# Performance work log

Hardware: AMD Instinct MI355X
Metric: run time of the kernel (lower is better)

## Reference

```python
import jax, jax.numpy as jnp
import numpy as np

EMBED_DIM = 1024
HEAD_SIZE = 64
SEQ_LEN = 2048
BATCH = 32

def setup_inputs() -> dict:
    key = jax.random.key(0)
    kx, kk, kq, kv = jax.random.split(key, 4)
    s = 1.0 / np.sqrt(EMBED_DIM)
    x = jax.random.normal(kx, (BATCH, SEQ_LEN, EMBED_DIM), dtype=jnp.float32)
    Wk = jax.random.normal(kk, (EMBED_DIM, HEAD_SIZE), dtype=jnp.float32) * s
    Wq = jax.random.normal(kq, (EMBED_DIM, HEAD_SIZE), dtype=jnp.float32) * s
    Wv = jax.random.normal(kv, (EMBED_DIM, HEAD_SIZE), dtype=jnp.float32) * s
    return {"x": x, "Wk": Wk, "Wq": Wq, "Wv": Wv}

def reference(x, Wk, Wq, Wv):
    # x: [B,T,C]; projections (no bias, per config.bias=False)
    k = jnp.einsum('btc,ch->bth', x, Wk)
    q = jnp.einsum('btc,ch->bth', x, Wq)
    v = jnp.einsum('btc,ch->bth', x, Wv)
    # NOTE: original computes k @ q^T (rows=k positions), scaled by embed_dim**-0.5
    scale = EMBED_DIM ** (-0.5)
    wei = jnp.einsum('bih,bjh->bij', k, q) * scale  # [B,T,T]
    T = x.shape[1]
    causal = jnp.tril(jnp.ones((T, T), dtype=bool))
    wei = jnp.where(causal, wei, -jnp.inf)
    wei = jax.nn.softmax(wei, axis=-1)
    # dropout: eval mode -> identity
    return jnp.einsum('bij,bjh->bih', wei, v)
```

## Files before the change

kernel.cpp:

```cpp
#include <hip/hip_runtime.h>
#include <hip/hip_bf16.h>

#define BATCH 32
#define SEQ   2048
#define EMB   1024
#define HS    64
#define BT    (BATCH*SEQ)

typedef short s16x4 __attribute__((ext_vector_type(4)));
typedef short s16x8 __attribute__((ext_vector_type(8)));
typedef float f32x4 __attribute__((ext_vector_type(4)));
using u16 = unsigned short;

static __device__ __forceinline__ short f2bf(float f) {
  __hip_bfloat16 h = __float2bfloat16(f);
  return *reinterpret_cast<short*>(&h);
}

#define MFMA __builtin_amdgcn_mfma_f32_16x16x32_bf16

__global__ __launch_bounds__(256) void wconv_kernel(
    const float* __restrict__ Wk, const float* __restrict__ Wq,
    const float* __restrict__ Wv, short* __restrict__ Wt)
{
  const int n = blockIdx.x;
  const int w = n >> 6, h = n & 63;
  const float* Wp = (w == 0) ? Wk : (w == 1) ? Wq : Wv;
  const int k0 = threadIdx.x * 4;
  s16x4 p;
  #pragma unroll
  for (int e = 0; e < 4; ++e) p[e] = f2bf(Wp[(size_t)(k0 + e) * HS + h]);
  *(s16x4*)(Wt + (size_t)n * EMB + k0) = p;
}

__global__ __launch_bounds__(256, 4) void proj_kernel(
    const float* __restrict__ x, const short* __restrict__ Wt,
    short* __restrict__ kb, short* __restrict__ qb, short* __restrict__ vt)
{
  __shared__ __align__(16) u16 xs[64][72];
  const int tid  = threadIdx.x;
  const int row0 = blockIdx.x * 64;
  const int w  = tid >> 6, l = tid & 63;
  const int lr = l & 15, lg = l >> 4;

  f32x4 acc[4][3];
  #pragma unroll
  for (int m = 0; m < 4; ++m)
    #pragma unroll
    for (int n = 0; n < 3; ++n) acc[m][n] = f32x4{0.f, 0.f, 0.f, 0.f};

  for (int k0 = 0; k0 < EMB; k0 += 64) {
    s16x8 bw[2][3];
    #pragma unroll
    for (int kk = 0; kk < 2; ++kk)
      #pragma unroll
      for (int n = 0; n < 3; ++n)
        bw[kk][n] = *(const s16x8*)(Wt + (size_t)(w*48 + n*16 + lr) * EMB + k0 + kk*32 + lg*8);
    __syncthreads();
    #pragma unroll
    for (int i = 0; i < 4; ++i) {
      const int idx = i * 256 + tid;
      const int r = idx >> 4, c4 = idx & 15;
      float4 t = *(const float4*)(x + (size_t)(row0 + r) * EMB + k0 + c4 * 4);
      s16x4 p;
      p[0] = f2bf(t.x); p[1] = f2bf(t.y); p[2] = f2bf(t.z); p[3] = f2bf(t.w);
      *(s16x4*)&xs[r][c4 * 4] = p;
    }
    __syncthreads();
    #pragma unroll
    for (int kk = 0; kk < 2; ++kk) {
      s16x8 a[4];
      #pragma unroll
      for (int m = 0; m < 4; ++m)
        a[m] = *(const s16x8*)&xs[m*16 + lr][kk*32 + lg*8];
      #pragma unroll
      for (int m = 0; m < 4; ++m)
        #pragma unroll
        for (int n = 0; n < 3; ++n)
          acc[m][n] = MFMA(a[m], bw[kk][n], acc[m][n], 0, 0, 0);
    }
  }

  const int b  = row0 >> 11;
  const int t0 = row0 & 2047;
  #pragma unroll
  for (int m = 0; m < 4; ++m) {
    const int trow = m*16 + lg*4;
    #pragma unroll
    for (int n = 0; n < 3; ++n) {
      const int nbase = w*48 + n*16;
      const int wm = nbase >> 6;
      const int h  = (nbase + lr) & 63;
      if (wm == 2) {
        s16x4 p;
        #pragma unroll
        for (int r = 0; r < 4; ++r) p[r] = f2bf(acc[m][n][r]);
        *(s16x4*)(vt + ((size_t)(b*64 + h)) * SEQ + t0 + trow) = p;
      } else {
        short* dst = (wm == 0) ? kb : qb;
        #pragma unroll
        for (int r = 0; r < 4; ++r)
          dst[(size_t)(row0 + trow + r) * HS + h] = f2bf(acc[m][n][r]);
      }
    }
  }
}

__global__ __launch_bounds__(256, 4) void attn_kernel(
    const short* __restrict__ kb, const short* __restrict__ qb,
    const short* __restrict__ vt, float* __restrict__ out)
{
  __shared__ __align__(16) u16 q_s[64*64];
  __shared__ __align__(16) u16 v_s[64*64];
  __shared__ __align__(16) u16 P_lds[4][16][72];
  const int bid = blockIdx.x;
  const int wg  = (bid & 7) * 128 + (bid >> 3);
  const int b   = wg >> 5;
  const int it  = 31 - (wg & 31);
  const int tid = threadIdx.x;
  const int w   = tid >> 6;
  const int lr  = tid & 15;
  const int lg  = (tid & 63) >> 4;
  const int iw0 = it * 64 + w * 16;

  const short* qbb = qb + (size_t)b * SEQ * HS;
  const short* vtb = vt + (size_t)b * 64 * SEQ;

  s16x8 ones;
  #pragma unroll
  for (int e = 0; e < 8; ++e) ones[e] = (short)0x3F80;

  s16x8 kfrag[2];
  {
    const short* kp = kb + ((size_t)(b*SEQ) + iw0 + lr) * HS + lg*8;
    kfrag[0] = *(const s16x8*)(kp);
    kfrag[1] = *(const s16x8*)(kp + 32);
  }

  f32x4 o[4];
  #pragma unroll
  for (int n = 0; n < 4; ++n) o[n] = f32x4{0.f, 0.f, 0.f, 0.f};
  f32x4 lac = f32x4{0.f, 0.f, 0.f, 0.f};

  #pragma unroll 1
  for (int jt = 0; jt <= it; ++jt) {
    const int j0 = jt * 64;
    __syncthreads();
    #pragma unroll
    for (int i = 0; i < 2; ++i) {
      const int idx = i * 256 + tid;
      const int row = idx >> 3, c8 = idx & 7;
      const int dst = row * 64 + ((c8 * 8) ^ ((row & 7) << 3));
      *(s16x8*)&q_s[dst] = *(const s16x8*)(qbb + (size_t)(j0 + row) * HS + c8 * 8);
      *(s16x8*)&v_s[dst] = *(const s16x8*)(vtb + (size_t)row * SEQ + j0 + c8 * 8);
    }
    __syncthreads();
    f32x4 sc[4];
    #pragma unroll
    for (int s = 0; s < 4; ++s) {
      const int row = s*16 + lr, base = row * 64, swz = (row & 7) << 3;
      s16x8 q0 = *(const s16x8*)&q_s[base + ((lg*8) ^ swz)];
      s16x8 q1 = *(const s16x8*)&q_s[base + ((32 + lg*8) ^ swz)];
      f32x4 z = f32x4{0.f, 0.f, 0.f, 0.f};
      z = MFMA(q0, kfrag[0], z, 0, 0, 0);
      z = MFMA(q1, kfrag[1], z, 0, 0, 0);
      sc[s] = z;
    }
    const bool diag = (jt == it);
    #pragma unroll
    for (int s = 0; s < 4; ++s) {
      s16x4 pk;
      #pragma unroll
      for (int r = 0; r < 4; ++r) {
        float e = __expf(fmaf(sc[s][r], 0.03125f, -4.0f));
        if (diag && (s*16 + lg*4 + r > w*16 + lr)) e = 0.f;
        pk[r] = f2bf(e);
      }
      *(s16x4*)&P_lds[w][lr][16*s + 4*lg] = pk;
    }
    s16x8 pA0 = *(const s16x8*)&P_lds[w][lr][8*lg];
    s16x8 pA1 = *(const s16x8*)&P_lds[w][lr][32 + 8*lg];
    __builtin_amdgcn_s_setprio(1);
    #pragma unroll
    for (int n = 0; n < 4; ++n) {
      const int rowh = n*16 + lr, base = rowh * 64, swz = (rowh & 7) << 3;
      s16x8 v0 = *(const s16x8*)&v_s[base + ((lg*8) ^ swz)];
      s16x8 v1 = *(const s16x8*)&v_s[base + ((32 + lg*8) ^ swz)];
      o[n] = MFMA(pA0, v0, o[n], 0, 0, 0);
      o[n] = MFMA(pA1, v1, o[n], 0, 0, 0);
    }
    lac = MFMA(pA0, ones, lac, 0, 0, 0);
    lac = MFMA(pA1, ones, lac, 0, 0, 0);
    __builtin_amdgcn_s_setprio(0);
  }

  float inv[4];
  #pragma unroll
  for (int r = 0; r < 4; ++r) inv[r] = 1.f / lac[r];
  #pragma unroll
  for (int n = 0; n < 4; ++n)
    #pragma unroll
    for (int r = 0; r < 4; ++r)
      out[((size_t)(b*SEQ) + iw0 + lg*4 + r) * HS + n*16 + lr] = o[n][r] * inv[r];
}

extern "C" void kernel_launch(void* const* d_in, const int* in_sizes, int n_in,
                              void* d_out, int out_size, void* d_ws, size_t ws_size,
                              hipStream_t stream) {
  const float* x  = (const float*)d_in[0];
  const float* Wk = (const float*)d_in[1];
  const float* Wq = (const float*)d_in[2];
  const float* Wv = (const float*)d_in[3];
  float* out = (float*)d_out;
  const size_t PLANE = (size_t)BT * HS;
  short* kb = (short*)d_ws;
  short* qb = kb + PLANE;
  short* vt = kb + 2*PLANE;
  short* Wt = kb + 3*PLANE;

  wconv_kernel<<<192, 256, 0, stream>>>(Wk, Wq, Wv, Wt);
  proj_kernel<<<BT/64, 256, 0, stream>>>(x, Wt, kb, qb, vt);
  attn_kernel<<<BATCH*(SEQ/64), 256, 0, stream>>>(kb, qb, vt, out);
}
```

Before: 136.1 us.

## Switch attention to 32x32 MFMA tiles with 128-row blocks and register P transpose

The attention kernel now uses 32x32x16 bf16 MFMAs, each wave owning 32 key rows, so a block covers 128 rows and each loaded q/v tile is reused by twice as many rows. The P matrix is converted from accumulator layout to operand layout in registers with v_permlane32_swap, which removes the LDS round trip for P. The aim is fewer LDS accesses, better MFMA efficiency and better tile reuse. In exchange, register pressure rises (launch bounds drop to 2 blocks per SIMD), the grid is halved, and some waves idle on the last tile because of the causal limit.

```diff
diff --git a/kernel.cpp b/kernel.cpp
--- a/kernel.cpp
+++ b/kernel.cpp
@@ -10,14 +10,23 @@
 typedef short s16x4 __attribute__((ext_vector_type(4)));
 typedef short s16x8 __attribute__((ext_vector_type(8)));
 typedef float f32x4 __attribute__((ext_vector_type(4)));
+typedef float f32x16 __attribute__((ext_vector_type(16)));
 using u16 = unsigned short;
+using u32 = unsigned int;
 
 static __device__ __forceinline__ short f2bf(float f) {
   __hip_bfloat16 h = __float2bfloat16(f);
   return *reinterpret_cast<short*>(&h);
 }
-
-#define MFMA __builtin_amdgcn_mfma_f32_16x16x32_bf16
+static __device__ __forceinline__ u32 pk2(float lo, float hi) {
+  return (u32)(u16)f2bf(lo) | ((u32)(u16)f2bf(hi) << 16);
+}
+static __device__ __forceinline__ void pl32swap(u32& a, u32& b) {
+  asm volatile("v_permlane32_swap_b32 %0, %1" : "+v"(a), "+v"(b));
+}
+
+#define MFMA   __builtin_amdgcn_mfma_f32_16x16x32_bf16
+#define MFMA32 __builtin_amdgcn_mfma_f32_32x32x16_bf16
 
 __global__ __launch_bounds__(256) void wconv_kernel(
     const float* __restrict__ Wk, const float* __restrict__ Wq,
@@ -106,22 +115,23 @@
   }
 }
 
-__global__ __launch_bounds__(256, 4) void attn_kernel(
+__global__ __launch_bounds__(256, 2) void attn_kernel(
     const short* __restrict__ kb, const short* __restrict__ qb,
     const short* __restrict__ vt, float* __restrict__ out)
 {
   __shared__ __align__(16) u16 q_s[64*64];
   __shared__ __align__(16) u16 v_s[64*64];
-  __shared__ __align__(16) u16 P_lds[4][16][72];
   const int bid = blockIdx.x;
-  const int wg  = (bid & 7) * 128 + (bid >> 3);
-  const int b   = wg >> 5;
-  const int it  = 31 - (wg & 31);
+  const int wg  = (bid & 7) * 64 + (bid >> 3);
+  const int b   = wg >> 4;
+  const int it  = 15 - (wg & 15);
   const int tid = threadIdx.x;
   const int w   = tid >> 6;
-  const int lr  = tid & 15;
-  const int lg  = (tid & 63) >> 4;
-  const int iw0 = it * 64 + w * 16;
+  const int l   = tid & 63;
+  const int li  = l & 31;
+  const int hi  = l >> 5;
+  const int iw0 = it * 128 + w * 32;
+  const int jlast = 2 * it + (w >> 1);
 
   const short* qbb = qb + (size_t)b * SEQ * HS;
   const short* vtb = vt + (size_t)b * 64 * SEQ;
@@ -130,78 +140,95 @@
   #pragma unroll
   for (int e = 0; e < 8; ++e) ones[e] = (short)0x3F80;
 
-  s16x8 kfrag[2];
-  {
-    const short* kp = kb + ((size_t)(b*SEQ) + iw0 + lr) * HS + lg*8;
-    kfrag[0] = *(const s16x8*)(kp);
-    kfrag[1] = *(const s16x8*)(kp + 32);
-  }
-
-  f32x4 o[4];
-  #pragma unroll
-  for (int n = 0; n < 4; ++n) o[n] = f32x4{0.f, 0.f, 0.f, 0.f};
-  f32x4 lac = f32x4{0.f, 0.f, 0.f, 0.f};
+  s16x8 kfrag[4];
+  #pragma unroll
+  for (int kst = 0; kst < 4; ++kst)
+    kfrag[kst] = *(const s16x8*)(kb + ((size_t)(b*SEQ) + iw0 + li) * HS + kst*16 + hi*8);
+
+  f32x16 o0, o1, lac;
+  #pragma unroll
+  for (int r = 0; r < 16; ++r) { o0[r] = 0.f; o1[r] = 0.f; lac[r] = 0.f; }
 
   #pragma unroll 1
-  for (int jt = 0; jt <= it; ++jt) {
+  for (int jt = 0; jt <= 2*it + 1; ++jt) {
     const int j0 = jt * 64;
     __syncthreads();
     #pragma unroll
-    for (int i = 0; i < 2; ++i) {
-      const int idx = i * 256 + tid;
+    for (int i2 = 0; i2 < 2; ++i2) {
+      const int idx = i2 * 256 + tid;
       const int row = idx >> 3, c8 = idx & 7;
       const int dst = row * 64 + ((c8 * 8) ^ ((row & 7) << 3));
       *(s16x8*)&q_s[dst] = *(const s16x8*)(qbb + (size_t)(j0 + row) * HS + c8 * 8);
       *(s16x8*)&v_s[dst] = *(const s16x8*)(vtb + (size_t)row * SEQ + j0 + c8 * 8);
     }
     __syncthreads();
-    f32x4 sc[4];
-    #pragma unroll
-    for (int s = 0; s < 4; ++s) {
-      const int row = s*16 + lr, base = row * 64, swz = (row & 7) << 3;
-      s16x8 q0 = *(const s16x8*)&q_s[base + ((lg*8) ^ swz)];
-      s16x8 q1 = *(const s16x8*)&q_s[base + ((32 + lg*8) ^ swz)];
-      f32x4 z = f32x4{0.f, 0.f, 0.f, 0.f};
-      z = MFMA(q0, kfrag[0], z, 0, 0, 0);
-      z = MFMA(q1, kfrag[1], z, 0, 0, 0);
-      sc[s] = z;
-    }
-    const bool diag = (jt == it);
-    #pragma unroll
-    for (int s = 0; s < 4; ++s) {
-      s16x4 pk;
-      #pragma unroll
-      for (int r = 0; r < 4; ++r) {
-        float e = __expf(fmaf(sc[s][r], 0.03125f, -4.0f));
-        if (diag && (s*16 + lg*4 + r > w*16 + lr)) e = 0.f;
-        pk[r] = f2bf(e);
+    if (jt > jlast) continue;
+
+    f32x16 s0, s1;
+    #pragma unroll
+    for (int r = 0; r < 16; ++r) { s0[r] = 0.f; s1[r] = 0.f; }
+    __builtin_amdgcn_s_setprio(1);
+    #pragma unroll
+    for (int kst = 0; kst < 4; ++kst) {
+      const int cswz = (kst*16 + hi*8) ^ ((li & 7) << 3);
+      s16x8 a0 = *(const s16x8*)&q_s[li * 64 + cswz];
+      s16x8 a1 = *(const s16x8*)&q_s[(32 + li) * 64 + cswz];
+      s0 = MFMA32(a0, kfrag[kst], s0, 0, 0, 0);
+      s1 = MFMA32(a1, kfrag[kst], s1, 0, 0, 0);
+    }
+    __builtin_amdgcn_s_setprio(0);
+
+    const bool maskT = (j0 + 63 > iw0);
+    const int  ig    = iw0 + li;
+    u32 pa[4][4];
+    #pragma unroll
+    for (int sub = 0; sub < 2; ++sub) {
+      float p[16];
+      #pragma unroll
+      for (int r = 0; r < 16; ++r) {
+        const float sv = sub ? s1[r] : s0[r];
+        float e = __expf(fmaf(sv, 0.03125f, -4.0f));
+        if (maskT) {
+          const int jg = j0 + sub*32 + (r & 3) + 8*(r >> 2) + 4*hi;
+          if (jg > ig) e = 0.f;
+        }
+        p[r] = e;
       }
-      *(s16x4*)&P_lds[w][lr][16*s + 4*lg] = pk;
-    }
-    s16x8 pA0 = *(const s16x8*)&P_lds[w][lr][8*lg];
-    s16x8 pA1 = *(const s16x8*)&P_lds[w][lr][32 + 8*lg];
+      #pragma unroll
+      for (int t = 0; t < 2; ++t) {
+        u32 a0 = pk2(p[t*8+0], p[t*8+1]);
+        u32 a1 = pk2(p[t*8+2], p[t*8+3]);
+        u32 b0 = pk2(p[t*8+4], p[t*8+5]);
+        u32 b1 = pk2(p[t*8+6], p[t*8+7]);
+        pl32swap(a0, b0);
+        pl32swap(a1, b1);
+        pa[sub*2 + t][0] = a0; pa[sub*2 + t][1] = a1;
+        pa[sub*2 + t][2] = b0; pa[sub*2 + t][3] = b1;
+      }
+    }
+
     __builtin_amdgcn_s_setprio(1);
     #pragma unroll
-    for (int n = 0; n < 4; ++n) {
-      const int rowh = n*16 + lr, base = rowh * 64, swz = (rowh & 7) << 3;
-      s16x8 v0 = *(const s16x8*)&v_s[base + ((lg*8) ^ swz)];
-      s16x8 v1 = *(const s16x8*)&v_s[base + ((32 + lg*8) ^ swz)];
-      o[n] = MFMA(pA0, v0, o[n], 0, 0, 0);
-      o[n] = MFMA(pA1, v1, o[n], 0, 0, 0);
-    }
-    lac = MFMA(pA0, ones, lac, 0, 0, 0);
-    lac = MFMA(pA1, ones, lac, 0, 0, 0);
+    for (int kst = 0; kst < 4; ++kst) {
+      const int cswz = (kst*16 + hi*8) ^ ((li & 7) << 3);
+      s16x8 v0 = *(const s16x8*)&v_s[li * 64 + cswz];
+      s16x8 v1 = *(const s16x8*)&v_s[(32 + li) * 64 + cswz];
+      s16x8 pf = *(const s16x8*)&pa[kst][0];
+      o0  = MFMA32(pf, v0, o0, 0, 0, 0);
+      o1  = MFMA32(pf, v1, o1, 0, 0, 0);
+      lac = MFMA32(pf, ones, lac, 0, 0, 0);
+    }
     __builtin_amdgcn_s_setprio(0);
   }
 
-  float inv[4];
-  #pragma unroll
-  for (int r = 0; r < 4; ++r) inv[r] = 1.f / lac[r];
-  #pragma unroll
-  for (int n = 0; n < 4; ++n)
-    #pragma unroll
-    for (int r = 0; r < 4; ++r)
-      out[((size_t)(b*SEQ) + iw0 + lg*4 + r) * HS + n*16 + lr] = o[n][r] * inv[r];
+  #pragma unroll
+  for (int r = 0; r < 16; ++r) {
+    const int row = iw0 + (r & 3) + 8*(r >> 2) + 4*hi;
+    const float inv = 1.f / lac[r];
+    float* op = out + ((size_t)(b*SEQ) + row) * HS + li;
+    op[0]  = o0[r] * inv;
+    op[32] = o1[r] * inv;
+  }
 }
 
 extern "C" void kernel_launch(void* const* d_in, const int* in_sizes, int n_in,
@@ -220,5 +247,5 @@
 
   wconv_kernel<<<192, 256, 0, stream>>>(Wk, Wq, Wv, Wt);
   proj_kernel<<<BT/64, 256, 0, stream>>>(x, Wt, kb, qb, vt);
-  attn_kernel<<<BATCH*(SEQ/64), 256, 0, stream>>>(kb, qb, vt, out);
-}
+  attn_kernel<<<BATCH*(SEQ/128), 256, 0, stream>>>(kb, qb, vt, out);
+}
```

After: 144.1 us. 5.9% more time.

## Double-buffer attention Q/V tiles with direct global-to-LDS async loads

Applied to the files above, without the earlier changes.

Replaces the synchronous register-staged copy of the Q and V^T tiles in the attention loop with global_load_lds into double-buffered shared memory. The next tile is prefetched while the current one is consumed, cutting the two barriers per iteration to one. LDS use roughly doubles, so launch bounds drop to 3 waves-per-EU, which may lower occupancy. The swizzle is applied on the global read side so that each wave's contiguous LDS writes land in the swizzled layout.

```diff
diff --git a/kernel.cpp b/kernel.cpp
--- a/kernel.cpp
+++ b/kernel.cpp
@@ -15,6 +15,11 @@
 static __device__ __forceinline__ short f2bf(float f) {
   __hip_bfloat16 h = __float2bfloat16(f);
   return *reinterpret_cast<short*>(&h);
+}
+static __device__ __forceinline__ void gl_lds16(const void* g, void* l) {
+  __builtin_amdgcn_global_load_lds(
+      (const __attribute__((address_space(1))) unsigned int*)g,
+      (__attribute__((address_space(3))) unsigned int*)l, 16, 0, 0);
 }
 
 #define MFMA __builtin_amdgcn_mfma_f32_16x16x32_bf16
@@ -106,12 +111,12 @@
   }
 }
 
-__global__ __launch_bounds__(256, 4) void attn_kernel(
+__global__ __launch_bounds__(256, 3) void attn_kernel(
     const short* __restrict__ kb, const short* __restrict__ qb,
     const short* __restrict__ vt, float* __restrict__ out)
 {
-  __shared__ __align__(16) u16 q_s[64*64];
-  __shared__ __align__(16) u16 v_s[64*64];
+  __shared__ __align__(16) u16 q_s[2][4096];
+  __shared__ __align__(16) u16 v_s[2][4096];
   __shared__ __align__(16) u16 P_lds[4][16][72];
   const int bid = blockIdx.x;
   const int wg  = (bid & 7) * 128 + (bid >> 3);
@@ -126,6 +131,22 @@
   const short* qbb = qb + (size_t)b * SEQ * HS;
   const short* vtb = vt + (size_t)b * 64 * SEQ;
 
+  const int srow0 = (0*256 + tid) >> 3, sc80 = tid & 7;
+  const int srow1 = (256 + tid) >> 3;
+  const int gcol0 = (sc80 * 8) ^ ((srow0 & 7) << 3);
+  const int gcol1 = (sc80 * 8) ^ ((srow1 & 7) << 3);
+
+#define STAGE(BUF, J0) do {                                                    \
+    u16* lq0 = &q_s[BUF][(w*64) * 8];                                          \
+    u16* lv0 = &v_s[BUF][(w*64) * 8];                                          \
+    u16* lq1 = &q_s[BUF][(256 + w*64) * 8];                                    \
+    u16* lv1 = &v_s[BUF][(256 + w*64) * 8];                                    \
+    gl_lds16(qbb + (size_t)((J0) + srow0) * HS + gcol0, lq0);                  \
+    gl_lds16(vtb + (size_t)srow0 * SEQ + (J0) + gcol0, lv0);                   \
+    gl_lds16(qbb + (size_t)((J0) + srow1) * HS + gcol1, lq1);                  \
+    gl_lds16(vtb + (size_t)srow1 * SEQ + (J0) + gcol1, lv1);                   \
+  } while (0)
+
   s16x8 ones;
   #pragma unroll
   for (int e = 0; e < 8; ++e) ones[e] = (short)0x3F80;
@@ -142,25 +163,21 @@
   for (int n = 0; n < 4; ++n) o[n] = f32x4{0.f, 0.f, 0.f, 0.f};
   f32x4 lac = f32x4{0.f, 0.f, 0.f, 0.f};
 
+  STAGE(0, 0);
+  __syncthreads();
+
+  int cur = 0;
   #pragma unroll 1
   for (int jt = 0; jt <= it; ++jt) {
-    const int j0 = jt * 64;
-    __syncthreads();
-    #pragma unroll
-    for (int i = 0; i < 2; ++i) {
-      const int idx = i * 256 + tid;
-      const int row = idx >> 3, c8 = idx & 7;
-      const int dst = row * 64 + ((c8 * 8) ^ ((row & 7) << 3));
-      *(s16x8*)&q_s[dst] = *(const s16x8*)(qbb + (size_t)(j0 + row) * HS + c8 * 8);
-      *(s16x8*)&v_s[dst] = *(const s16x8*)(vtb + (size_t)row * SEQ + j0 + c8 * 8);
-    }
-    __syncthreads();
+    if (jt < it) STAGE(cur ^ 1, (jt + 1) * 64);
+    const u16* qsb = q_s[cur];
+    const u16* vsb = v_s[cur];
     f32x4 sc[4];
     #pragma unroll
     for (int s = 0; s < 4; ++s) {
       const int row = s*16 + lr, base = row * 64, swz = (row & 7) << 3;
-      s16x8 q0 = *(const s16x8*)&q_s[base + ((lg*8) ^ swz)];
-      s16x8 q1 = *(const s16x8*)&q_s[base + ((32 + lg*8) ^ swz)];
+      s16x8 q0 = *(const s16x8*)&qsb[base + ((lg*8) ^ swz)];
+      s16x8 q1 = *(const s16x8*)&qsb[base + ((32 + lg*8) ^ swz)];
       f32x4 z = f32x4{0.f, 0.f, 0.f, 0.f};
       z = MFMA(q0, kfrag[0], z, 0, 0, 0);
       z = MFMA(q1, kfrag[1], z, 0, 0, 0);
@@ -184,15 +201,18 @@
     #pragma unroll
     for (int n = 0; n < 4; ++n) {
       const int rowh = n*16 + lr, base = rowh * 64, swz = (rowh & 7) << 3;
-      s16x8 v0 = *(const s16x8*)&v_s[base + ((lg*8) ^ swz)];
-      s16x8 v1 = *(const s16x8*)&v_s[base + ((32 + lg*8) ^ swz)];
+      s16x8 v0 = *(const s16x8*)&vsb[base + ((lg*8) ^ swz)];
+      s16x8 v1 = *(const s16x8*)&vsb[base + ((32 + lg*8) ^ swz)];
       o[n] = MFMA(pA0, v0, o[n], 0, 0, 0);
       o[n] = MFMA(pA1, v1, o[n], 0, 0, 0);
     }
     lac = MFMA(pA0, ones, lac, 0, 0, 0);
     lac = MFMA(pA1, ones, lac, 0, 0, 0);
     __builtin_amdgcn_s_setprio(0);
-  }
+    __syncthreads();
+    cur ^= 1;
+  }
+#undef STAGE
 
   float inv[4];
   #pragma unroll
```

New measurement: 129.3 us. 1.05x faster.
